# Optimization experiments

Hardware: AMD Instinct MI355X
Metric: run time of the kernel (lower is better)

The kernel has to match this reference:

```python
import jax, jax.numpy as jnp
import numpy as np

B, N, K, C = 8, 4096, 2048, 256


def setup_inputs() -> dict:
    key = jax.random.key(0)
    kx, ka, kp = jax.random.split(key, 3)
    x = jax.random.normal(kx, (B, K, C), dtype=jnp.float32)
    A = jax.random.uniform(ka, (B, N, N), dtype=jnp.float32)
    # idx mask with EXACTLY K ones per batch row (TopKPool keeps a fixed count)
    perms = jax.vmap(lambda k: jax.random.permutation(k, N))(jax.random.split(kp, B))
    idx = jnp.zeros((B, N), dtype=jnp.int32).at[jnp.arange(B)[:, None], perms[:, :K]].set(1)
    return {"x": x, "idx": idx, "A": A}


def reference(x, idx, A):
    # x: [B, K, C] pooled features; idx: [B, N] 0/1 selection mask; A: [B, N, N] (only N is used)
    b, k, c = x.shape
    n = A.shape[1]
    mask = idx > 0
    # Stable argsort puts the (exactly k) selected positions first, in increasing node order,
    # matching tf.where's ordering of nonzero indices.
    order = jnp.argsort(jnp.where(mask, 0, 1), axis=1, stable=True)  # [B, N]
    sel = order[:, :k]  # [B, K] node positions to receive the pooled features
    out = jnp.zeros((b, n, c), dtype=x.dtype)
    out = out.at[jnp.arange(b)[:, None], sel].set(x)  # single batched parallel scatter
    return out
```

## Files before the change

kernel.cpp:

```cpp
#include <hip/hip_runtime.h>

#define BB 8
#define NN 4096
#define KK 2048
#define CC 256

__global__ __launch_bounds__(256) void topk_fused_kernel(const float4* __restrict__ x,
                                                         const int* __restrict__ idx,
                                                         float4* __restrict__ out) {
    const int bi = blockIdx.x;
    const int b = bi >> 10;
    const int rowStart = (bi & 1023) * 4;
    const int t = threadIdx.x;
    const int lane = t & 63;
    const int wave = t >> 6;

    const int* idxB = idx + (size_t)b * NN;
    const int4* idxB4 = (const int4*)idxB;

    int partial = 0;
    const int n4 = rowStart >> 2;
    for (int i = t; i < n4; i += 256) {
        int4 v = idxB4[i];
        partial += v.x + v.y + v.z + v.w;
    }
#pragma unroll
    for (int off = 32; off > 0; off >>= 1)
        partial += __shfl_down(partial, off, 64);

    __shared__ int waveSum[4];
    if (lane == 0) waveSum[wave] = partial;
    __syncthreads();
    const int base = waveSum[0] + waveSum[1] + waveSum[2] + waveSum[3];

    const int4 v4 = idxB4[rowStart >> 2];
    const int myIdx = (wave == 0) ? v4.x : (wave == 1) ? v4.y : (wave == 2) ? v4.z : v4.w;
    const int pre = ((wave > 0) ? v4.x : 0) + ((wave > 1) ? v4.y : 0) + ((wave > 2) ? v4.z : 0);

    const long long row = (long long)b * NN + rowStart + wave;
    float4 val = make_float4(0.f, 0.f, 0.f, 0.f);
    if (myIdx > 0) {
        const int r = base + pre;
        val = x[((long long)b * KK + r) * (CC / 4) + lane];
    }
    out[row * (CC / 4) + lane] = val;
}

extern "C" void kernel_launch(void* const* d_in, const int* in_sizes, int n_in,
                              void* d_out, int out_size, void* d_ws, size_t ws_size,
                              hipStream_t stream) {
    const float* x  = (const float*)d_in[0];
    const int* idx  = (const int*)d_in[1];
    float* out = (float*)d_out;

    topk_fused_kernel<<<(BB * NN) / 4, 256, 0, stream>>>(
        (const float4*)x, idx, (float4*)out);
}
```

Baseline: 15.43 us.

## Process 64 rows per 1024-thread block with shared prefix scan and nontemporal copies

```diff
diff --git a/kernel.cpp b/kernel.cpp
--- a/kernel.cpp
+++ b/kernel.cpp
@@ -3,14 +3,16 @@
 #define BB 8
 #define NN 4096
 #define KK 2048
-#define CC 256
+#define C4 64
 
-__global__ __launch_bounds__(256) void topk_fused_kernel(const float4* __restrict__ x,
-                                                         const int* __restrict__ idx,
-                                                         float4* __restrict__ out) {
+typedef float f32x4 __attribute__((ext_vector_type(4)));
+
+__global__ __launch_bounds__(1024) void topk_fused_kernel(const f32x4* __restrict__ x,
+                                                          const int* __restrict__ idx,
+                                                          f32x4* __restrict__ out) {
     const int bi = blockIdx.x;
-    const int b = bi >> 10;
-    const int rowStart = (bi & 1023) * 4;
+    const int b = bi >> 6;
+    const int rowStart = (bi & 63) << 6;
     const int t = threadIdx.x;
     const int lane = t & 63;
     const int wave = t >> 6;
@@ -18,32 +20,48 @@
     const int* idxB = idx + (size_t)b * NN;
     const int4* idxB4 = (const int4*)idxB;
 
+    __shared__ int waveSum[16];
+    __shared__ int pref[64];
+    __shared__ int idxs[64];
+
     int partial = 0;
     const int n4 = rowStart >> 2;
-    for (int i = t; i < n4; i += 256) {
-        int4 v = idxB4[i];
-        partial += v.x + v.y + v.z + v.w;
+    if (t < n4) {
+        int4 v = idxB4[t];
+        partial = v.x + v.y + v.z + v.w;
     }
 #pragma unroll
     for (int off = 32; off > 0; off >>= 1)
         partial += __shfl_down(partial, off, 64);
+    if (lane == 0) waveSum[wave] = partial;
 
-    __shared__ int waveSum[4];
-    if (lane == 0) waveSum[wave] = partial;
+    if (wave == 0) {
+        const int myv = idxB[rowStart + lane];
+        idxs[lane] = myv;
+        int incl = myv;
+#pragma unroll
+        for (int off = 1; off < 64; off <<= 1) {
+            int up = __shfl_up(incl, off, 64);
+            if (lane >= off) incl += up;
+        }
+        pref[lane] = incl - myv;
+    }
     __syncthreads();
-    const int base = waveSum[0] + waveSum[1] + waveSum[2] + waveSum[3];
 
-    const int4 v4 = idxB4[rowStart >> 2];
-    const int myIdx = (wave == 0) ? v4.x : (wave == 1) ? v4.y : (wave == 2) ? v4.z : v4.w;
-    const int pre = ((wave > 0) ? v4.x : 0) + ((wave > 1) ? v4.y : 0) + ((wave > 2) ? v4.z : 0);
+    int base = 0;
+#pragma unroll
+    for (int w = 0; w < 16; ++w) base += waveSum[w];
 
-    const long long row = (long long)b * NN + rowStart + wave;
-    float4 val = make_float4(0.f, 0.f, 0.f, 0.f);
-    if (myIdx > 0) {
-        const int r = base + pre;
-        val = x[((long long)b * KK + r) * (CC / 4) + lane];
+    const long long outRow0 = (long long)b * NN + rowStart;
+    const long long xBase = (long long)b * KK + base;
+#pragma unroll
+    for (int r = 0; r < 4; ++r) {
+        const int rib = wave * 4 + r;
+        f32x4 val = (f32x4)(0.f);
+        if (idxs[rib] > 0)
+            val = __builtin_nontemporal_load(&x[(xBase + pref[rib]) * C4 + lane]);
+        __builtin_nontemporal_store(val, &out[(outRow0 + rib) * C4 + lane]);
     }
-    out[row * (CC / 4) + lane] = val;
 }
 
 extern "C" void kernel_launch(void* const* d_in, const int* in_sizes, int n_in,
@@ -53,6 +71,6 @@
     const int* idx  = (const int*)d_in[1];
     float* out = (float*)d_out;
 
-    topk_fused_kernel<<<(BB * NN) / 4, 256, 0, stream>>>(
-        (const float4*)x, idx, (float4*)out);
+    topk_fused_kernel<<<(BB * NN) / 64, 1024, 0, stream>>>(
+        (const f32x4*)x, idx, (f32x4*)out);
 }
```

Result: slower. 17.34 us (+12.4%).
